# Kernel tuning notes

Hardware: AMD Instinct MI355X
Metric: run time of the kernel (lower is better)

Reference implementation:

```python
import jax, jax.numpy as jnp
import numpy as np

B, T, D, H = 512, 256, 81, 128


def setup_inputs() -> dict:
    key = jax.random.key(0)
    ks = jax.random.split(key, 10)
    s = lambda *sh: 1.0 / np.sqrt(sh[-1])
    X_input = jax.random.normal(ks[0], (B, T, D), dtype=jnp.float32)
    # attention MLP: Linear(2H -> H), Tanh, Linear(H -> D)
    W1 = jax.random.uniform(ks[1], (H, 2 * H), jnp.float32, -s(2 * H), s(2 * H))
    b1 = jax.random.uniform(ks[2], (H,), jnp.float32, -s(2 * H), s(2 * H))
    W2 = jax.random.uniform(ks[3], (D, H), jnp.float32, -s(H), s(H))
    b2 = jax.random.uniform(ks[4], (D,), jnp.float32, -s(H), s(H))
    # single-layer LSTM, PyTorch gate order (i, f, g, o)
    W_ih = jax.random.uniform(ks[5], (4 * H, D), jnp.float32, -s(H), s(H))
    W_hh = jax.random.uniform(ks[6], (4 * H, H), jnp.float32, -s(H), s(H))
    b_ih = jax.random.uniform(ks[7], (4 * H,), jnp.float32, -s(H), s(H))
    b_hh = jax.random.uniform(ks[8], (4 * H,), jnp.float32, -s(H), s(H))
    return {"X_input": X_input, "W1": W1, "b1": b1, "W2": W2, "b2": b2,
            "W_ih": W_ih, "W_hh": W_hh, "b_ih": b_ih, "b_hh": b_hh}


def reference(X_input, W1, b1, W2, b2, W_ih, W_hh, b_ih, b_hh):
    h0 = jnp.zeros((X_input.shape[0], H), X_input.dtype)
    c0 = jnp.zeros((X_input.shape[0], H), X_input.dtype)

    def step(carry, x_t):  # x_t: [B, D]
        h, c = carry
        # input-attention MLP on cat(h_{t-1}, s_{t-1})
        hs = jnp.concatenate([h, c], axis=1)                       # [B, 2H]
        e = jnp.tanh(hs @ W1.T + b1) @ W2.T + b2                   # [B, D]
        alpha = jax.nn.softmax(e, axis=1)                          # [B, D]
        xw = alpha * x_t                                           # [B, D]
        # single LSTM cell step (PyTorch gate order i, f, g, o)
        gates = xw @ W_ih.T + b_ih + h @ W_hh.T + b_hh             # [B, 4H]
        i, f, g, o = jnp.split(gates, 4, axis=1)
        c_new = jax.nn.sigmoid(f) * c + jax.nn.sigmoid(i) * jnp.tanh(g)
        h_new = jax.nn.sigmoid(o) * jnp.tanh(c_new)
        return (h_new, c_new), (h_new, alpha)

    (_, _), (hs, alphas) = jax.lax.scan(step, (h0, c0), jnp.swapaxes(X_input, 0, 1))
    encoder_hidden_states = jnp.swapaxes(hs, 0, 1)   # [B, T, H]
    all_alpha_t = jnp.swapaxes(alphas, 0, 1)         # [B, T, D]
    return encoder_hidden_states, all_alpha_t
```

## Files before the change

kernel.cpp:

```cpp
#include <hip/hip_runtime.h>
#include <math.h>

#define BB 512
#define TT 256
#define DD 81
#define HH 128

typedef _Float16 half8 __attribute__((ext_vector_type(8)));
typedef float    f32x4 __attribute__((ext_vector_type(4)));

#define BLOB_LDS_ELEMS 5632
#define BLOB_W4_ELEMS  14336
#define BLOB_W4_OFF    BLOB_LDS_ELEMS
#define WS_ELEMS       (BLOB_LDS_ELEMS + BLOB_W4_ELEMS)

#define W2_OFF   0
#define HS_OFF   24576
#define A1_OFF   25600
#define E_OFF    26112
#define ACT_OFF  26880
#define LDS_BYTES 27776

__device__ __forceinline__ float wave_sum(float v) {
#pragma unroll
    for (int off = 32; off > 0; off >>= 1) v += __shfl_xor(v, off, 64);
    return v;
}
__device__ __forceinline__ float wave_max(float v) {
#pragma unroll
    for (int off = 32; off > 0; off >>= 1) v = fmaxf(v, __shfl_xor(v, off, 64));
    return v;
}
__device__ __forceinline__ float fast_sig(float x)  { return 1.f / (1.f + __expf(-x)); }
__device__ __forceinline__ float fast_tanh(float x) { return 1.f - 2.f / (__expf(2.f * x) + 1.f); }

__device__ __forceinline__ float4 pack8h(const float* v) {
    union { float4 f4; _Float16 h[8]; } u;
#pragma unroll
    for (int c = 0; c < 8; ++c) u.h[c] = (_Float16)v[c];
    return u.f4;
}

__global__ void repack_lds_blob(const float* __restrict__ W1, const float* __restrict__ W2,
                                float4* __restrict__ dst) {
    int tid = blockIdx.x * blockDim.x + threadIdx.x;
    if (tid >= BLOB_LDS_ELEMS) return;
    float v[8];
    if (tid < 4096) {
        int c = tid >> 6, l = tid & 63;
        int nt = c >> 3, kt = c & 7;
        int n = 16 * nt + (l & 15);
        int kb = 32 * kt + ((l >> 4) << 3);
#pragma unroll
        for (int c2 = 0; c2 < 8; ++c2) v[c2] = W1[(size_t)n * 256 + kb + c2];
    } else {
        int idx = tid - 4096;
        int c = idx >> 6, l = idx & 63;
        int nt = c >> 2, kt = c & 3;
        int n = 16 * nt + (l & 15);
        int kb = 32 * kt + ((l >> 4) << 3);
#pragma unroll
        for (int c2 = 0; c2 < 8; ++c2)
            v[c2] = (n < 81) ? W2[(size_t)n * 128 + kb + c2] : 0.f;
    }
    dst[tid] = pack8h(v);
}

__global__ void repack_w4(const float* __restrict__ Wih, const float* __restrict__ Whh,
                          const float* __restrict__ bih, const float* __restrict__ bhh,
                          float4* __restrict__ dst) {
    int tid = blockIdx.x * blockDim.x + threadIdx.x;
    if (tid >= BLOB_W4_ELEMS) return;
    int f = tid >> 9, r = tid & 511;
    int w = r >> 6, l = r & 63;
    int j = f / 7, kt = f - 7 * j;
    int n = 128 * j + 16 * w + (l & 15);
    int kb = 32 * kt + ((l >> 4) << 3);
    float v[8];
#pragma unroll
    for (int c = 0; c < 8; ++c) {
        int k = kb + c;
        float x;
        if (k < 81)        x = Wih[(size_t)n * 81 + k];
        else if (k < 209)  x = Whh[(size_t)n * 128 + (k - 81)];
        else if (k == 209) x = bih[n] + bhh[n];
        else               x = 0.f;
        v[c] = x;
    }
    dst[tid] = pack8h(v);
}

__global__ __launch_bounds__(512, 2)
void encoder_kernel(const float* __restrict__ X,
                    const float* __restrict__ b1, const float* __restrict__ b2,
                    const float4* __restrict__ wlds, const float4* __restrict__ w4q,
                    float* __restrict__ out_h, float* __restrict__ out_alpha) {
    const int tid = threadIdx.x;
    const int w   = tid >> 6;
    const int l   = tid & 63;
    const int b0  = blockIdx.x * 2;

    __shared__ __align__(16) unsigned char lds[LDS_BYTES];

#pragma unroll
    for (int i = 0; i < 3; ++i)
        ((float4*)lds)[i * 512 + tid] = wlds[4096 + i * 512 + tid];

    half8 wb1[8];
#pragma unroll
    for (int kt = 0; kt < 8; ++kt) {
        float4 tt = wlds[(w * 8 + kt) * 64 + l];
        wb1[kt] = *(half8*)&tt;
    }

    half8 wf[4][7];
#pragma unroll
    for (int j = 0; j < 4; ++j)
#pragma unroll
        for (int kt = 0; kt < 7; ++kt) {
            float4 tt = w4q[(j * 7 + kt) * 512 + tid];
            wf[j][kt] = *(half8*)&tt;
        }

    const float breg1 = b1[16 * w + (l & 15)];
    const int   n2    = 16 * w + (l & 15);
    const float breg2 = (n2 < 81) ? b2[n2] : 0.f;

    if (tid < 512) ((unsigned short*)(lds + HS_OFF))[tid] = 0;
    if (tid < 448) {
        ((_Float16*)(lds + ACT_OFF))[tid] = ((tid % 224) == 209) ? (_Float16)1.0f
                                                                 : (_Float16)0.0f;
    }
    float c0 = 0.f, c1 = 0.f;
    __syncthreads();

#pragma unroll 1
    for (int t = 0; t < TT; ++t) {
        float xv0 = 0.f, xv1 = 0.f;
        if (w < 2) {
            const float* xr = X + ((size_t)(b0 + w) * TT + t) * DD;
            xv0 = xr[l];
            if (l < DD - 64) xv1 = xr[l + 64];
        }

        {
            const unsigned offA = HS_OFF + (l & 1) * 512 + (l >> 4) * 16;
            f32x4 ae = {0.f, 0.f, 0.f, 0.f}, ao = {0.f, 0.f, 0.f, 0.f};
#pragma unroll
            for (int kt = 0; kt < 8; ++kt) {
                half8 a = *(const half8*)(lds + offA + kt * 64);
                if (kt & 1) ao = __builtin_amdgcn_mfma_f32_16x16x32_f16(a, wb1[kt], ao, 0, 0, 0);
                else        ae = __builtin_amdgcn_mfma_f32_16x16x32_f16(a, wb1[kt], ae, 0, 0, 0);
            }
            if (l < 16) {
                _Float16* a1f = (_Float16*)(lds + A1_OFF);
                a1f[16 * w + l]       = (_Float16)fast_tanh(ae[0] + ao[0] + breg1);
                a1f[128 + 16 * w + l] = (_Float16)fast_tanh(ae[1] + ao[1] + breg1);
            }
        }
        __syncthreads();

        if (w < 6) {
            const unsigned offA = (l & 1) * 256 + (l >> 4) * 16;
            f32x4 ae = {0.f, 0.f, 0.f, 0.f}, ao = {0.f, 0.f, 0.f, 0.f};
#pragma unroll
            for (int kt = 0; kt < 4; ++kt) {
                half8 a = *(const half8*)(lds + A1_OFF + offA + kt * 64);
                half8 b = *(const half8*)(lds + W2_OFF + (w * 4 + kt) * 1024 + l * 16);
                if (kt & 1) ao = __builtin_amdgcn_mfma_f32_16x16x32_f16(a, b, ao, 0, 0, 0);
                else        ae = __builtin_amdgcn_mfma_f32_16x16x32_f16(a, b, ae, 0, 0, 0);
            }
            if (l < 16) {
                float* es = (float*)(lds + E_OFF);
                es[16 * w + l]      = ae[0] + ao[0] + breg2;
                es[96 + 16 * w + l] = ae[1] + ao[1] + breg2;
            }
        }
        __syncthreads();

        if (w < 2) {
            const float* er = (const float*)(lds + E_OFF) + w * 96;
            float ev0 = er[l];
            float ev1 = (l < DD - 64) ? er[l + 64] : -INFINITY;
            float m  = wave_max(fmaxf(ev0, ev1));
            float p0 = __expf(ev0 - m);
            float p1 = (l < DD - 64) ? __expf(ev1 - m) : 0.f;
            float inv = 1.f / wave_sum(p0 + p1);
            _Float16* act = (_Float16*)(lds + ACT_OFF) + w * 224;
            float* oa = out_alpha + ((size_t)(b0 + w) * TT + t) * DD;
            float al0 = p0 * inv;
            act[l] = (_Float16)(al0 * xv0);
            oa[l] = al0;
            if (l < DD - 64) {
                float al1 = p1 * inv;
                act[l + 64] = (_Float16)(al1 * xv1);
                oa[l + 64] = al1;
            }
        }
        __syncthreads();

        f32x4 g0 = {0.f,0.f,0.f,0.f}, g1 = g0, g2 = g0, g3 = g0;
        {
            const unsigned offA = ACT_OFF + (l & 1) * 448 + (l >> 4) * 16;
            half8 a4[7];
#pragma unroll
            for (int kt = 0; kt < 7; ++kt)
                a4[kt] = *(const half8*)(lds + offA + kt * 64);
#pragma unroll
            for (int kt = 0; kt < 7; ++kt) {
                g0 = __builtin_amdgcn_mfma_f32_16x16x32_f16(a4[kt], wf[0][kt], g0, 0, 0, 0);
                g1 = __builtin_amdgcn_mfma_f32_16x16x32_f16(a4[kt], wf[1][kt], g1, 0, 0, 0);
                g2 = __builtin_amdgcn_mfma_f32_16x16x32_f16(a4[kt], wf[2][kt], g2, 0, 0, 0);
                g3 = __builtin_amdgcn_mfma_f32_16x16x32_f16(a4[kt], wf[3][kt], g3, 0, 0, 0);
            }
        }
        __syncthreads();

        if (l < 16) {
            const int u = 16 * w + l;
            float cn0 = fast_sig(g1[0]) * c0 + fast_sig(g0[0]) * fast_tanh(g2[0]);
            float hn0 = fast_sig(g3[0]) * fast_tanh(cn0);
            c0 = cn0;
            float cn1 = fast_sig(g1[1]) * c1 + fast_sig(g0[1]) * fast_tanh(g2[1]);
            float hn1 = fast_sig(g3[1]) * fast_tanh(cn1);
            c1 = cn1;
            _Float16* hsp = (_Float16*)(lds + HS_OFF);
            hsp[u]             = (_Float16)hn0;
            hsp[128 + u]       = (_Float16)cn0;
            hsp[256 + u]       = (_Float16)hn1;
            hsp[256 + 128 + u] = (_Float16)cn1;
            _Float16* actp = (_Float16*)(lds + ACT_OFF);
            actp[81 + u]       = (_Float16)hn0;
            actp[224 + 81 + u] = (_Float16)hn1;
            out_h[((size_t)(b0 + 0) * TT + t) * HH + u] = hn0;
            out_h[((size_t)(b0 + 1) * TT + t) * HH + u] = hn1;
        }
        __syncthreads();
    }
}

extern "C" void kernel_launch(void* const* d_in, const int* in_sizes, int n_in,
                              void* d_out, int out_size, void* d_ws, size_t ws_size,
                              hipStream_t stream) {
    const float* X   = (const float*)d_in[0];
    const float* W1  = (const float*)d_in[1];
    const float* b1  = (const float*)d_in[2];
    const float* W2  = (const float*)d_in[3];
    const float* b2  = (const float*)d_in[4];
    const float* Wih = (const float*)d_in[5];
    const float* Whh = (const float*)d_in[6];
    const float* bih = (const float*)d_in[7];
    const float* bhh = (const float*)d_in[8];

    if (ws_size < (size_t)WS_ELEMS * sizeof(float4)) return;

    float4* blob = (float4*)d_ws;
    float4* wlds = blob;
    float4* w4q  = blob + BLOB_W4_OFF;

    repack_lds_blob<<<(BLOB_LDS_ELEMS + 255) / 256, 256, 0, stream>>>(W1, W2, wlds);
    repack_w4<<<(BLOB_W4_ELEMS + 255) / 256, 256, 0, stream>>>(Wih, Whh, bih, bhh, w4q);

    float* out_h     = (float*)d_out;
    float* out_alpha = (float*)d_out + (size_t)BB * TT * HH;

    encoder_kernel<<<BB / 2, 512, 0, stream>>>(X, b1, b2, wlds, w4q, out_h, out_alpha);
}
```

Baseline: 756.2 us.

## Fuse W2 projection with softmax, prefetch X, move W1 to LDS

Two waves (one per batch row) now each compute all six N-tiles of the W2 projection and run the softmax in registers with 16-lane shuffles. This removes the E buffer round-trip and one block barrier per timestep. X for the next step is prefetched into registers during the current step, and the LSTM cell update is spread over 32 lanes instead of 16. W1 fragments move from registers into LDS, raising LDS use to about 92KB, which may limit occupancy and adds LDS reads on every step.

```diff
diff --git a/kernel.cpp b/kernel.cpp
--- a/kernel.cpp
+++ b/kernel.cpp
@@ -14,23 +14,13 @@
 #define BLOB_W4_OFF    BLOB_LDS_ELEMS
 #define WS_ELEMS       (BLOB_LDS_ELEMS + BLOB_W4_ELEMS)
 
-#define W2_OFF   0
-#define HS_OFF   24576
-#define A1_OFF   25600
-#define E_OFF    26112
-#define ACT_OFF  26880
-#define LDS_BYTES 27776
-
-__device__ __forceinline__ float wave_sum(float v) {
-#pragma unroll
-    for (int off = 32; off > 0; off >>= 1) v += __shfl_xor(v, off, 64);
-    return v;
-}
-__device__ __forceinline__ float wave_max(float v) {
-#pragma unroll
-    for (int off = 32; off > 0; off >>= 1) v = fmaxf(v, __shfl_xor(v, off, 64));
-    return v;
-}
+#define W1_OFF   0
+#define W2_OFF   65536
+#define HS_OFF   90112
+#define A1_OFF   91136
+#define ACT_OFF  91648
+#define LDS_BYTES 92544
+
 __device__ __forceinline__ float fast_sig(float x)  { return 1.f / (1.f + __expf(-x)); }
 __device__ __forceinline__ float fast_tanh(float x) { return 1.f - 2.f / (__expf(2.f * x) + 1.f); }
 
@@ -103,15 +93,8 @@
     __shared__ __align__(16) unsigned char lds[LDS_BYTES];
 
 #pragma unroll
-    for (int i = 0; i < 3; ++i)
-        ((float4*)lds)[i * 512 + tid] = wlds[4096 + i * 512 + tid];
-
-    half8 wb1[8];
-#pragma unroll
-    for (int kt = 0; kt < 8; ++kt) {
-        float4 tt = wlds[(w * 8 + kt) * 64 + l];
-        wb1[kt] = *(half8*)&tt;
-    }
+    for (int i = 0; i < 11; ++i)
+        ((float4*)lds)[i * 512 + tid] = wlds[i * 512 + tid];
 
     half8 wf[4][7];
 #pragma unroll
@@ -123,34 +106,42 @@
         }
 
     const float breg1 = b1[16 * w + (l & 15)];
-    const int   n2    = 16 * w + (l & 15);
-    const float breg2 = (n2 < 81) ? b2[n2] : 0.f;
+    float b2v[6];
+#pragma unroll
+    for (int nt = 0; nt < 6; ++nt) {
+        int n = 16 * nt + (l & 15);
+        b2v[nt] = (n < DD) ? b2[n] : -INFINITY;
+    }
 
     if (tid < 512) ((unsigned short*)(lds + HS_OFF))[tid] = 0;
     if (tid < 448) {
         ((_Float16*)(lds + ACT_OFF))[tid] = ((tid % 224) == 209) ? (_Float16)1.0f
                                                                  : (_Float16)0.0f;
     }
-    float c0 = 0.f, c1 = 0.f;
+    float creg = 0.f;
+
+    float xr[6];
+    if (w < 2) {
+        const float* xp = X + ((size_t)(b0 + w) * TT + 0) * DD;
+#pragma unroll
+        for (int nt = 0; nt < 6; ++nt) {
+            int n = 16 * nt + (l & 15);
+            xr[nt] = (n < DD) ? xp[n] : 0.f;
+        }
+    }
     __syncthreads();
 
 #pragma unroll 1
     for (int t = 0; t < TT; ++t) {
-        float xv0 = 0.f, xv1 = 0.f;
-        if (w < 2) {
-            const float* xr = X + ((size_t)(b0 + w) * TT + t) * DD;
-            xv0 = xr[l];
-            if (l < DD - 64) xv1 = xr[l + 64];
-        }
-
         {
             const unsigned offA = HS_OFF + (l & 1) * 512 + (l >> 4) * 16;
             f32x4 ae = {0.f, 0.f, 0.f, 0.f}, ao = {0.f, 0.f, 0.f, 0.f};
 #pragma unroll
             for (int kt = 0; kt < 8; ++kt) {
                 half8 a = *(const half8*)(lds + offA + kt * 64);
-                if (kt & 1) ao = __builtin_amdgcn_mfma_f32_16x16x32_f16(a, wb1[kt], ao, 0, 0, 0);
-                else        ae = __builtin_amdgcn_mfma_f32_16x16x32_f16(a, wb1[kt], ae, 0, 0, 0);
+                half8 b = *(const half8*)(lds + W1_OFF + (w * 8 + kt) * 1024 + l * 16);
+                if (kt & 1) ao = __builtin_amdgcn_mfma_f32_16x16x32_f16(a, b, ao, 0, 0, 0);
+                else        ae = __builtin_amdgcn_mfma_f32_16x16x32_f16(a, b, ae, 0, 0, 0);
             }
             if (l < 16) {
                 _Float16* a1f = (_Float16*)(lds + A1_OFF);
@@ -160,41 +151,59 @@
         }
         __syncthreads();
 
-        if (w < 6) {
-            const unsigned offA = (l & 1) * 256 + (l >> 4) * 16;
-            f32x4 ae = {0.f, 0.f, 0.f, 0.f}, ao = {0.f, 0.f, 0.f, 0.f};
-#pragma unroll
-            for (int kt = 0; kt < 4; ++kt) {
-                half8 a = *(const half8*)(lds + A1_OFF + offA + kt * 64);
-                half8 b = *(const half8*)(lds + W2_OFF + (w * 4 + kt) * 1024 + l * 16);
-                if (kt & 1) ao = __builtin_amdgcn_mfma_f32_16x16x32_f16(a, b, ao, 0, 0, 0);
-                else        ae = __builtin_amdgcn_mfma_f32_16x16x32_f16(a, b, ae, 0, 0, 0);
-            }
+        if (w < 2) {
+            half8 a2[4];
+#pragma unroll
+            for (int kt = 0; kt < 4; ++kt)
+                a2[kt] = *(const half8*)(lds + A1_OFF + (l & 1) * 256 + (l >> 4) * 16 + kt * 64);
+            f32x4 acc[6];
+#pragma unroll
+            for (int nt = 0; nt < 6; ++nt) acc[nt] = (f32x4){0.f, 0.f, 0.f, 0.f};
+#pragma unroll
+            for (int kt = 0; kt < 4; ++kt)
+#pragma unroll
+                for (int nt = 0; nt < 6; ++nt) {
+                    half8 bfr = *(const half8*)(lds + W2_OFF + (nt * 4 + kt) * 1024 + l * 16);
+                    acc[nt] = __builtin_amdgcn_mfma_f32_16x16x32_f16(a2[kt], bfr, acc[nt], 0, 0, 0);
+                }
+            float e[6];
+#pragma unroll
+            for (int nt = 0; nt < 6; ++nt) {
+                float v = (w == 0) ? acc[nt][0] : acc[nt][1];
+                e[nt] = v + b2v[nt];
+            }
+            float m = fmaxf(fmaxf(fmaxf(e[0], e[1]), fmaxf(e[2], e[3])), fmaxf(e[4], e[5]));
+            m = fmaxf(m, __shfl_xor(m, 1, 64));
+            m = fmaxf(m, __shfl_xor(m, 2, 64));
+            m = fmaxf(m, __shfl_xor(m, 4, 64));
+            m = fmaxf(m, __shfl_xor(m, 8, 64));
+            float p[6], s = 0.f;
+#pragma unroll
+            for (int nt = 0; nt < 6; ++nt) { p[nt] = __expf(e[nt] - m); s += p[nt]; }
+            s += __shfl_xor(s, 1, 64);
+            s += __shfl_xor(s, 2, 64);
+            s += __shfl_xor(s, 4, 64);
+            s += __shfl_xor(s, 8, 64);
+            float inv = 1.f / s;
             if (l < 16) {
-                float* es = (float*)(lds + E_OFF);
-                es[16 * w + l]      = ae[0] + ao[0] + breg2;
-                es[96 + 16 * w + l] = ae[1] + ao[1] + breg2;
-            }
-        }
-        __syncthreads();
-
-        if (w < 2) {
-            const float* er = (const float*)(lds + E_OFF) + w * 96;
-            float ev0 = er[l];
-            float ev1 = (l < DD - 64) ? er[l + 64] : -INFINITY;
-            float m  = wave_max(fmaxf(ev0, ev1));
-            float p0 = __expf(ev0 - m);
-            float p1 = (l < DD - 64) ? __expf(ev1 - m) : 0.f;
-            float inv = 1.f / wave_sum(p0 + p1);
-            _Float16* act = (_Float16*)(lds + ACT_OFF) + w * 224;
-            float* oa = out_alpha + ((size_t)(b0 + w) * TT + t) * DD;
-            float al0 = p0 * inv;
-            act[l] = (_Float16)(al0 * xv0);
-            oa[l] = al0;
-            if (l < DD - 64) {
-                float al1 = p1 * inv;
-                act[l + 64] = (_Float16)(al1 * xv1);
-                oa[l + 64] = al1;
+                _Float16* act = (_Float16*)(lds + ACT_OFF) + w * 224;
+                float* oa = out_alpha + ((size_t)(b0 + w) * TT + t) * DD;
+#pragma unroll
+                for (int nt = 0; nt < 6; ++nt) {
+                    int n = 16 * nt + l;
+                    if (n < DD) {
+                        float al = p[nt] * inv;
+                        act[n] = (_Float16)(al * xr[nt]);
+                        oa[n]  = al;
+                    }
+                }
+            }
+            int tn = (t + 1 < TT) ? t + 1 : t;
+            const float* xp = X + ((size_t)(b0 + w) * TT + tn) * DD;
+#pragma unroll
+            for (int nt = 0; nt < 6; ++nt) {
+                int n = 16 * nt + (l & 15);
+                xr[nt] = (n < DD) ? xp[n] : 0.f;
             }
         }
         __syncthreads();
@@ -216,24 +225,21 @@
         }
         __syncthreads();
 
-        if (l < 16) {
-            const int u = 16 * w + l;
-            float cn0 = fast_sig(g1[0]) * c0 + fast_sig(g0[0]) * fast_tanh(g2[0]);
-            float hn0 = fast_sig(g3[0]) * fast_tanh(cn0);
-            c0 = cn0;
-            float cn1 = fast_sig(g1[1]) * c1 + fast_sig(g0[1]) * fast_tanh(g2[1]);
-            float hn1 = fast_sig(g3[1]) * fast_tanh(cn1);
-            c1 = cn1;
+        if (l < 32) {
+            const int r = l >> 4;
+            const int u = 16 * w + (l & 15);
+            float gi = r ? g0[1] : g0[0];
+            float gf = r ? g1[1] : g1[0];
+            float gg = r ? g2[1] : g2[0];
+            float go = r ? g3[1] : g3[0];
+            float cn = fast_sig(gf) * creg + fast_sig(gi) * fast_tanh(gg);
+            float hn = fast_sig(go) * fast_tanh(cn);
+            creg = cn;
             _Float16* hsp = (_Float16*)(lds + HS_OFF);
-            hsp[u]             = (_Float16)hn0;
-            hsp[128 + u]       = (_Float16)cn0;
-            hsp[256 + u]       = (_Float16)hn1;
-            hsp[256 + 128 + u] = (_Float16)cn1;
-            _Float16* actp = (_Float16*)(lds + ACT_OFF);
-            actp[81 + u]       = (_Float16)hn0;
-            actp[224 + 81 + u] = (_Float16)hn1;
-            out_h[((size_t)(b0 + 0) * TT + t) * HH + u] = hn0;
-            out_h[((size_t)(b0 + 1) * TT + t) * HH + u] = hn1;
+            hsp[r * 256 + u]       = (_Float16)hn;
+            hsp[r * 256 + 128 + u] = (_Float16)cn;
+            ((_Float16*)(lds + ACT_OFF))[r * 224 + 81 + u] = (_Float16)hn;
+            out_h[((size_t)(b0 + r) * TT + t) * HH + u] = hn;
         }
         __syncthreads();
     }
```

Measured after the change: 810.5 us. +7.2%, slower.

## Process one batch row per block and double the grid size

Applied to the files above, without the earlier changes.

Each block now handles a single batch row instead of two, so the grid doubles to 512 blocks. The launch bound is raised to request four resident blocks per CU. The aim is to spread the latency-bound recurrence over more concurrent blocks, with LDS buffers shrunk to match. The cost is that each MFMA now fills only one of its 16 A rows. The higher occupancy target may also force the register-resident weight fragments to spill.

```diff
diff --git a/kernel.cpp b/kernel.cpp
--- a/kernel.cpp
+++ b/kernel.cpp
@@ -16,10 +16,10 @@
 
 #define W2_OFF   0
 #define HS_OFF   24576
-#define A1_OFF   25600
-#define E_OFF    26112
-#define ACT_OFF  26880
-#define LDS_BYTES 27776
+#define A1_OFF   25088
+#define E_OFF    25344
+#define ACT_OFF  25728
+#define LDS_BYTES 26176
 
 __device__ __forceinline__ float wave_sum(float v) {
 #pragma unroll
@@ -90,7 +90,7 @@
     dst[tid] = pack8h(v);
 }
 
-__global__ __launch_bounds__(512, 2)
+__global__ __launch_bounds__(512, 4)
 void encoder_kernel(const float* __restrict__ X,
                     const float* __restrict__ b1, const float* __restrict__ b2,
                     const float4* __restrict__ wlds, const float4* __restrict__ w4q,
@@ -98,7 +98,7 @@
     const int tid = threadIdx.x;
     const int w   = tid >> 6;
     const int l   = tid & 63;
-    const int b0  = blockIdx.x * 2;
+    const int b   = blockIdx.x;
 
     __shared__ __align__(16) unsigned char lds[LDS_BYTES];
 
@@ -126,25 +126,24 @@
     const int   n2    = 16 * w + (l & 15);
     const float breg2 = (n2 < 81) ? b2[n2] : 0.f;
 
-    if (tid < 512) ((unsigned short*)(lds + HS_OFF))[tid] = 0;
-    if (tid < 448) {
-        ((_Float16*)(lds + ACT_OFF))[tid] = ((tid % 224) == 209) ? (_Float16)1.0f
-                                                                 : (_Float16)0.0f;
-    }
-    float c0 = 0.f, c1 = 0.f;
+    if (tid < 256) ((unsigned short*)(lds + HS_OFF))[tid] = 0;
+    if (tid < 224) {
+        ((_Float16*)(lds + ACT_OFF))[tid] = (tid == 209) ? (_Float16)1.0f : (_Float16)0.0f;
+    }
+    float creg = 0.f;
     __syncthreads();
 
 #pragma unroll 1
     for (int t = 0; t < TT; ++t) {
         float xv0 = 0.f, xv1 = 0.f;
-        if (w < 2) {
-            const float* xr = X + ((size_t)(b0 + w) * TT + t) * DD;
-            xv0 = xr[l];
-            if (l < DD - 64) xv1 = xr[l + 64];
+        if (w == 0) {
+            const float* xp = X + ((size_t)b * TT + t) * DD;
+            xv0 = xp[l];
+            if (l < DD - 64) xv1 = xp[l + 64];
         }
 
         {
-            const unsigned offA = HS_OFF + (l & 1) * 512 + (l >> 4) * 16;
+            const unsigned offA = HS_OFF + (l >> 4) * 16;
             f32x4 ae = {0.f, 0.f, 0.f, 0.f}, ao = {0.f, 0.f, 0.f, 0.f};
 #pragma unroll
             for (int kt = 0; kt < 8; ++kt) {
@@ -154,40 +153,36 @@
             }
             if (l < 16) {
                 _Float16* a1f = (_Float16*)(lds + A1_OFF);
-                a1f[16 * w + l]       = (_Float16)fast_tanh(ae[0] + ao[0] + breg1);
-                a1f[128 + 16 * w + l] = (_Float16)fast_tanh(ae[1] + ao[1] + breg1);
+                a1f[16 * w + l] = (_Float16)fast_tanh(ae[0] + ao[0] + breg1);
             }
         }
         __syncthreads();
 
         if (w < 6) {
-            const unsigned offA = (l & 1) * 256 + (l >> 4) * 16;
+            const unsigned offA = (l >> 4) * 16;
             f32x4 ae = {0.f, 0.f, 0.f, 0.f}, ao = {0.f, 0.f, 0.f, 0.f};
 #pragma unroll
             for (int kt = 0; kt < 4; ++kt) {
                 half8 a = *(const half8*)(lds + A1_OFF + offA + kt * 64);
-                half8 b = *(const half8*)(lds + W2_OFF + (w * 4 + kt) * 1024 + l * 16);
-                if (kt & 1) ao = __builtin_amdgcn_mfma_f32_16x16x32_f16(a, b, ao, 0, 0, 0);
-                else        ae = __builtin_amdgcn_mfma_f32_16x16x32_f16(a, b, ae, 0, 0, 0);
-            }
-            if (l < 16) {
-                float* es = (float*)(lds + E_OFF);
-                es[16 * w + l]      = ae[0] + ao[0] + breg2;
-                es[96 + 16 * w + l] = ae[1] + ao[1] + breg2;
-            }
-        }
-        __syncthreads();
-
-        if (w < 2) {
-            const float* er = (const float*)(lds + E_OFF) + w * 96;
+                half8 bf = *(const half8*)(lds + W2_OFF + (w * 4 + kt) * 1024 + l * 16);
+                if (kt & 1) ao = __builtin_amdgcn_mfma_f32_16x16x32_f16(a, bf, ao, 0, 0, 0);
+                else        ae = __builtin_amdgcn_mfma_f32_16x16x32_f16(a, bf, ae, 0, 0, 0);
+            }
+            if (l < 16)
+                ((float*)(lds + E_OFF))[16 * w + l] = ae[0] + ao[0] + breg2;
+        }
+        __syncthreads();
+
+        if (w == 0) {
+            const float* er = (const float*)(lds + E_OFF);
             float ev0 = er[l];
             float ev1 = (l < DD - 64) ? er[l + 64] : -INFINITY;
             float m  = wave_max(fmaxf(ev0, ev1));
             float p0 = __expf(ev0 - m);
             float p1 = (l < DD - 64) ? __expf(ev1 - m) : 0.f;
             float inv = 1.f / wave_sum(p0 + p1);
-            _Float16* act = (_Float16*)(lds + ACT_OFF) + w * 224;
-            float* oa = out_alpha + ((size_t)(b0 + w) * TT + t) * DD;
+            _Float16* act = (_Float16*)(lds + ACT_OFF);
+            float* oa = out_alpha + ((size_t)b * TT + t) * DD;
             float al0 = p0 * inv;
             act[l] = (_Float16)(al0 * xv0);
             oa[l] = al0;
@@ -201,7 +196,7 @@
 
         f32x4 g0 = {0.f,0.f,0.f,0.f}, g1 = g0, g2 = g0, g3 = g0;
         {
-            const unsigned offA = ACT_OFF + (l & 1) * 448 + (l >> 4) * 16;
+            const unsigned offA = ACT_OFF + (l >> 4) * 16;
             half8 a4[7];
 #pragma unroll
             for (int kt = 0; kt < 7; ++kt)
@@ -218,22 +213,14 @@
 
         if (l < 16) {
             const int u = 16 * w + l;
-            float cn0 = fast_sig(g1[0]) * c0 + fast_sig(g0[0]) * fast_tanh(g2[0]);
-            float hn0 = fast_sig(g3[0]) * fast_tanh(cn0);
-            c0 = cn0;
-            float cn1 = fast_sig(g1[1]) * c1 + fast_sig(g0[1]) * fast_tanh(g2[1]);
-            float hn1 = fast_sig(g3[1]) * fast_tanh(cn1);
-            c1 = cn1;
+            float cn = fast_sig(g1[0]) * creg + fast_sig(g0[0]) * fast_tanh(g2[0]);
+            float hn = fast_sig(g3[0]) * fast_tanh(cn);
+            creg = cn;
             _Float16* hsp = (_Float16*)(lds + HS_OFF);
-            hsp[u]             = (_Float16)hn0;
-            hsp[128 + u]       = (_Float16)cn0;
-            hsp[256 + u]       = (_Float16)hn1;
-            hsp[256 + 128 + u] = (_Float16)cn1;
-            _Float16* actp = (_Float16*)(lds + ACT_OFF);
-            actp[81 + u]       = (_Float16)hn0;
-            actp[224 + 81 + u] = (_Float16)hn1;
-            out_h[((size_t)(b0 + 0) * TT + t) * HH + u] = hn0;
-            out_h[((size_t)(b0 + 1) * TT + t) * HH + u] = hn1;
+            hsp[u]       = (_Float16)hn;
+            hsp[128 + u] = (_Float16)cn;
+            ((_Float16*)(lds + ACT_OFF))[81 + u] = (_Float16)hn;
+            out_h[((size_t)b * TT + t) * HH + u] = hn;
         }
         __syncthreads();
     }
@@ -264,5 +251,5 @@
     float* out_h     = (float*)d_out;
     float* out_alpha = (float*)d_out + (size_t)BB * TT * HH;
 
-    encoder_kernel<<<BB / 2, 512, 0, stream>>>(X, b1, b2, wlds, w4q, out_h, out_alpha);
-}
+    encoder_kernel<<<BB, 512, 0, stream>>>(X, b1, b2, wlds, w4q, out_h, out_alpha);
+}
```

Result: slower. 2.563 ms (+238.9%).
